# Kernel optimization log

Hardware: AMD Instinct MI355X
Metric: run time of the kernel (lower is better)

The kernel has to match this reference:

```python
import jax, jax.numpy as jnp
import numpy as np

T, B, IN_DIM, D_VALUE, D_KEY = 1024, 8, 512, 64, 64
EPS = 1e-8

def setup_inputs() -> dict:
    key = jax.random.key(0)
    ks = jax.random.split(key, 7)
    s = 1.0 / np.sqrt(IN_DIM)
    return {
        "x":  jax.random.normal(ks[0], (T, B, IN_DIM), dtype=jnp.float32),
        "Wv": jax.random.uniform(ks[1], (D_VALUE, IN_DIM), jnp.float32, -s, s),
        "bv": jax.random.uniform(ks[2], (D_VALUE,), jnp.float32, -s, s),
        "Wk": jax.random.uniform(ks[3], (D_KEY, IN_DIM), jnp.float32, -s, s),
        "bk": jax.random.uniform(ks[4], (D_KEY,), jnp.float32, -s, s),
        "Wa": jax.random.uniform(ks[5], (D_KEY, IN_DIM), jnp.float32, -s, s),
        "ba": jax.random.uniform(ks[6], (D_KEY,), jnp.float32, -s, s),
    }

def reference(x, Wv, bv, Wk, bk, Wa, ba):
    # Projections: x (T,B,in_dim) -> v (T,B,d), k (T,B,n), alpha (T,B,n)
    v = jnp.einsum('tbi,di->tbd', x, Wv) + bv
    k = jnp.einsum('tbi,ni->tbn', x, Wk) + bk
    alpha = jax.nn.sigmoid(jnp.einsum('tbi,ni->tbn', x, Wa) + ba)
    # outer product per timestep: (T,B,d,n)
    outer = jnp.einsum('tbd,tbn->tbdn', v, k)
    # log-space cumulative decay, normalized by final cumprod
    log_cumprod = jnp.cumsum(jnp.log(jnp.maximum(alpha, EPS)), axis=0)  # (T,B,n)
    cumprod = jnp.exp(log_cumprod)
    decay = cumprod / (cumprod[-1:] + EPS)
    weighted = outer * decay[:, :, None, :]  # (T,B,d,n)
    S = jnp.cumsum(weighted, axis=0)
    return S
```

## Files before the change

### kernel.cpp

```cpp
#include <hip/hip_runtime.h>
#include <math.h>

#define T_DIM  1024
#define B_DIM  8
#define IN_D   512
#define NROWS  (T_DIM * B_DIM)
#define EPSF   1e-8f

#define CHUNK  16
#define NCHUNK (T_DIM / CHUNK)
#define SEG    16
#define NSEG   (T_DIM / SEG)

typedef float vfloat4 __attribute__((ext_vector_type(4)));

#define OFF_WT   0
#define OFF_V    (OFF_WT + IN_D * 192)
#define OFF_K    (OFF_V  + NROWS * 64)
#define OFF_Z    (OFF_K  + NROWS * 64)
#define OFF_SEG  (OFF_Z  + NROWS * 64)
#define OFF_TOT  (OFF_SEG + NSEG * B_DIM * 64)
#define OFF_P    (OFF_TOT + B_DIM * 64)

__global__ void k0_wt(const float* __restrict__ Wv, const float* __restrict__ Wk,
                      const float* __restrict__ Wa, float* __restrict__ Wt) {
    int idx = blockIdx.x * 256 + threadIdx.x;
    int i = idx / 192, c = idx % 192;
    float v;
    if (c < 64)       v = Wv[c * IN_D + i];
    else if (c < 128) v = Wk[(c - 64) * IN_D + i];
    else              v = Wa[(c - 128) * IN_D + i];
    Wt[i * 192 + c] = v;
}

__global__ __launch_bounds__(256) void k1_proj(
        const float* __restrict__ x, const float* __restrict__ Wt,
        const float* __restrict__ bv, const float* __restrict__ bk, const float* __restrict__ ba,
        float* __restrict__ V, float* __restrict__ Kb, float* __restrict__ Zb) {
    __shared__ float xs[2][32][32];
    __shared__ float wsm[2][32][192];
    const int tid  = threadIdx.x;
    const int h    = tid >> 7;
    const int t7   = tid & 127;
    const int rq   = t7 >> 4;
    const int cq   = t7 & 15;
    const int row0 = blockIdx.x * 32;

    float4 acc[4][3];
#pragma unroll
    for (int j = 0; j < 4; ++j)
#pragma unroll
        for (int m = 0; m < 3; ++m) acc[j][m] = make_float4(0.f, 0.f, 0.f, 0.f);

    for (int s = 0; s < 8; ++s) {
#pragma unroll
        for (int q = 0; q < 2; ++q) {
            int idx = tid + q * 256;
            int hh = idx >> 8, r = idx & 31, f = (idx >> 5) & 7;
            float4 v4 = reinterpret_cast<const float4*>(x)[((row0 + r) * IN_D + hh * 256 + s * 32 + f * 4) >> 2];
            xs[hh][f * 4 + 0][r] = v4.x;
            xs[hh][f * 4 + 1][r] = v4.y;
            xs[hh][f * 4 + 2][r] = v4.z;
            xs[hh][f * 4 + 3][r] = v4.w;
        }
#pragma unroll
        for (int q = 0; q < 12; ++q) {
            int idx = tid + q * 256;
            int hh = idx / 1536;
            int rem = idx - hh * 1536;
            int kk = rem / 48;
            int f  = rem - kk * 48;
            float4 v4 = reinterpret_cast<const float4*>(Wt)[((hh * 256 + s * 32 + kk) * 192 + f * 4) >> 2];
            *reinterpret_cast<float4*>(&wsm[hh][kk][f * 4]) = v4;
        }
        __syncthreads();

#pragma unroll 4
        for (int kk = 0; kk < 32; ++kk) {
            float4 xv = *reinterpret_cast<const float4*>(&xs[h][kk][rq * 4]);
#pragma unroll
            for (int m = 0; m < 3; ++m) {
                float4 wq = *reinterpret_cast<const float4*>(&wsm[h][kk][m * 64 + cq * 4]);
#pragma unroll
                for (int j = 0; j < 4; ++j) {
                    float xx = (&xv.x)[j];
                    acc[j][m].x = fmaf(xx, wq.x, acc[j][m].x);
                    acc[j][m].y = fmaf(xx, wq.y, acc[j][m].y);
                    acc[j][m].z = fmaf(xx, wq.z, acc[j][m].z);
                    acc[j][m].w = fmaf(xx, wq.w, acc[j][m].w);
                }
            }
        }
        __syncthreads();
    }

    float* red = &wsm[0][0][0];
    if (h == 1) {
#pragma unroll
        for (int j = 0; j < 4; ++j)
#pragma unroll
            for (int m = 0; m < 3; ++m)
                *reinterpret_cast<float4*>(&red[t7 * 52 + (j * 3 + m) * 4]) = acc[j][m];
    }
    __syncthreads();
    if (h == 0) {
        float4 bv4 = *reinterpret_cast<const float4*>(&bv[cq * 4]);
        float4 bk4 = *reinterpret_cast<const float4*>(&bk[cq * 4]);
        float4 ba4 = *reinterpret_cast<const float4*>(&ba[cq * 4]);
#pragma unroll
        for (int j = 0; j < 4; ++j) {
            int row = row0 + rq * 4 + j;
#pragma unroll
            for (int m = 0; m < 3; ++m) {
                float4 o = *reinterpret_cast<const float4*>(&red[t7 * 52 + (j * 3 + m) * 4]);
                o.x += (&acc[j][m].x)[0];
                o.x = acc[j][m].x + (&o.x)[0] - acc[j][m].x;
            }
            float4 o0 = *reinterpret_cast<const float4*>(&red[t7 * 52 + (j * 3 + 0) * 4]);
            float4 o1 = *reinterpret_cast<const float4*>(&red[t7 * 52 + (j * 3 + 1) * 4]);
            float4 o2 = *reinterpret_cast<const float4*>(&red[t7 * 52 + (j * 3 + 2) * 4]);
            float4 r0, r1, r2;
            r0.x = acc[j][0].x + o0.x + bv4.x; r0.y = acc[j][0].y + o0.y + bv4.y;
            r0.z = acc[j][0].z + o0.z + bv4.z; r0.w = acc[j][0].w + o0.w + bv4.w;
            r1.x = acc[j][1].x + o1.x + bk4.x; r1.y = acc[j][1].y + o1.y + bk4.y;
            r1.z = acc[j][1].z + o1.z + bk4.z; r1.w = acc[j][1].w + o1.w + bk4.w;
            r2.x = acc[j][2].x + o2.x + ba4.x; r2.y = acc[j][2].y + o2.y + ba4.y;
            r2.z = acc[j][2].z + o2.z + ba4.z; r2.w = acc[j][2].w + o2.w + ba4.w;
            *reinterpret_cast<float4*>(&V [row * 64 + cq * 4]) = r0;
            *reinterpret_cast<float4*>(&Kb[row * 64 + cq * 4]) = r1;
            *reinterpret_cast<float4*>(&Zb[row * 64 + cq * 4]) = r2;
        }
    }
}

__global__ void k2a_logs(float* __restrict__ Z, float* __restrict__ seg) {
    int b = blockIdx.x & 7, s = blockIdx.x >> 3;
    int n = threadIdx.x;
    int base = b * 64 + n;
    float accv = 0.f;
#pragma unroll
    for (int i = 0; i < SEG; ++i) {
        int t = s * SEG + i;
        float z = Z[t * 512 + base];
        float a = 1.f / (1.f + expf(-z));
        float l = logf(fmaxf(a, EPSF));
        Z[t * 512 + base] = l;
        accv += l;
    }
    seg[s * 512 + base] = accv;
}

__global__ void k2b_scan(float* __restrict__ seg, float* __restrict__ tot) {
    int i = threadIdx.x;
    float vals[NSEG];
#pragma unroll
    for (int s = 0; s < NSEG; ++s) vals[s] = seg[s * 512 + i];
    float run = 0.f;
#pragma unroll
    for (int s = 0; s < NSEG; ++s) { seg[s * 512 + i] = run; run += vals[s]; }
    tot[i] = run;
}

__global__ void k2c_w(const float* __restrict__ Z, const float* __restrict__ seg,
                      const float* __restrict__ tot, float* __restrict__ Kb) {
    int b = blockIdx.x & 7, s = blockIdx.x >> 3;
    int n = threadIdx.x;
    int base = b * 64 + n;
    float run = seg[s * 512 + base];
    float invden = 1.f / (expf(tot[base]) + EPSF);
#pragma unroll
    for (int i = 0; i < SEG; ++i) {
        int t = s * SEG + i;
        run += Z[t * 512 + base];
        Kb[t * 512 + base] *= expf(run) * invden;
    }
}

__global__ __launch_bounds__(256) void k3_partial(const float* __restrict__ V,
                                                  const float* __restrict__ W,
                                                  float* __restrict__ P) {
    __shared__ float vs[CHUNK * 64];
    __shared__ float wsh[CHUNK * 64];
    int b = blockIdx.x & 7, cch = blockIdx.x >> 3;
    int tid = threadIdx.x;
    int dg = tid >> 4, n4 = tid & 15;
    {
        int il = tid >> 4, f = tid & 15;
        int row = (cch * CHUNK + il) * 8 + b;
        reinterpret_cast<float4*>(vs)[il * 16 + f]  = reinterpret_cast<const float4*>(V)[row * 16 + f];
        reinterpret_cast<float4*>(wsh)[il * 16 + f] = reinterpret_cast<const float4*>(W)[row * 16 + f];
    }
    __syncthreads();
    float4 acc[4];
#pragma unroll
    for (int q = 0; q < 4; ++q) acc[q] = make_float4(0.f, 0.f, 0.f, 0.f);

#pragma unroll
    for (int i = 0; i < CHUNK; ++i) {
        float4 wv = reinterpret_cast<const float4*>(wsh)[i * 16 + n4];
#pragma unroll
        for (int q = 0; q < 4; ++q) {
            float vd = vs[i * 64 + dg + 16 * q];
            acc[q].x = fmaf(vd, wv.x, acc[q].x);
            acc[q].y = fmaf(vd, wv.y, acc[q].y);
            acc[q].z = fmaf(vd, wv.z, acc[q].z);
            acc[q].w = fmaf(vd, wv.w, acc[q].w);
        }
    }
    float* Pp = P + (cch * 8 + b) * 4096;
#pragma unroll
    for (int q = 0; q < 4; ++q)
        *reinterpret_cast<float4*>(Pp + (dg + 16 * q) * 64 + 4 * n4) = acc[q];
}

__global__ __launch_bounds__(256) void k4_prefix(float* __restrict__ P) {
    int gid = blockIdx.x * 256 + threadIdx.x;
    int b = gid >> 12, dn = gid & 4095;
    float run = 0.f;
#pragma unroll
    for (int c = 0; c < NCHUNK; ++c) {
        float v = P[(c * 8 + b) * 4096 + dn];
        P[(c * 8 + b) * 4096 + dn] = run;
        run += v;
    }
}

__global__ __launch_bounds__(256) void k5_main(const float* __restrict__ V,
                                               const float* __restrict__ W,
                                               const float* __restrict__ P,
                                               float* __restrict__ S) {
    __shared__ float vs[CHUNK * 64];
    __shared__ float wsh[CHUNK * 64];
    int b = blockIdx.x & 7, cch = blockIdx.x >> 3;
    int tid = threadIdx.x;
    int dg = tid >> 4, n4 = tid & 15;
    {
        int il = tid >> 4, f = tid & 15;
        int row = (cch * CHUNK + il) * 8 + b;
        reinterpret_cast<float4*>(vs)[il * 16 + f]  = reinterpret_cast<const float4*>(V)[row * 16 + f];
        reinterpret_cast<float4*>(wsh)[il * 16 + f] = reinterpret_cast<const float4*>(W)[row * 16 + f];
    }
    vfloat4 acc[4];
    const float* Pp = P + (cch * 8 + b) * 4096;
#pragma unroll
    for (int q = 0; q < 4; ++q)
        acc[q] = *reinterpret_cast<const vfloat4*>(Pp + (dg + 16 * q) * 64 + 4 * n4);
    __syncthreads();

#pragma unroll
    for (int i = 0; i < CHUNK; ++i) {
        float4 wv = reinterpret_cast<const float4*>(wsh)[i * 16 + n4];
        int t = cch * CHUNK + i;
        float* Sb = S + (size_t)t * 32768 + b * 4096;
#pragma unroll
        for (int q = 0; q < 4; ++q) {
            float vd = vs[i * 64 + dg + 16 * q];
            acc[q].x = fmaf(vd, wv.x, acc[q].x);
            acc[q].y = fmaf(vd, wv.y, acc[q].y);
            acc[q].z = fmaf(vd, wv.z, acc[q].z);
            acc[q].w = fmaf(vd, wv.w, acc[q].w);
            __builtin_nontemporal_store(acc[q],
                reinterpret_cast<vfloat4*>(Sb + (dg + 16 * q) * 64 + 4 * n4));
        }
    }
}

extern "C" void kernel_launch(void* const* d_in, const int* in_sizes, int n_in,
                              void* d_out, int out_size, void* d_ws, size_t ws_size,
                              hipStream_t stream) {
    const float* x  = (const float*)d_in[0];
    const float* Wv = (const float*)d_in[1];
    const float* bv = (const float*)d_in[2];
    const float* Wk = (const float*)d_in[3];
    const float* bk = (const float*)d_in[4];
    const float* Wa = (const float*)d_in[5];
    const float* ba = (const float*)d_in[6];
    float* S  = (float*)d_out;
    float* ws = (float*)d_ws;

    float* Wt  = ws + OFF_WT;
    float* V   = ws + OFF_V;
    float* Kb  = ws + OFF_K;
    float* Zb  = ws + OFF_Z;
    float* seg = ws + OFF_SEG;
    float* tot = ws + OFF_TOT;
    float* P   = ws + OFF_P;

    k0_wt     <<<384, 256, 0, stream>>>(Wv, Wk, Wa, Wt);
    k1_proj   <<<256, 256, 0, stream>>>(x, Wt, bv, bk, ba, V, Kb, Zb);
    k2a_logs  <<<512,  64, 0, stream>>>(Zb, seg);
    k2b_scan  <<<  1, 512, 0, stream>>>(seg, tot);
    k2c_w     <<<512,  64, 0, stream>>>(Zb, seg, tot, Kb);
    k3_partial<<<512, 256, 0, stream>>>(V, Kb, P);
    k4_prefix <<<128, 256, 0, stream>>>(P);
    k5_main   <<<512, 256, 0, stream>>>(V, Kb, P, S);
}
```

Baseline: 213.7 us.

## Fuse log-sigmoid and decay scan into projection and chunk kernels

```diff
diff --git a/kernel.cpp b/kernel.cpp
--- a/kernel.cpp
+++ b/kernel.cpp
@@ -6,6 +6,7 @@
 #define IN_D   512
 #define NROWS  (T_DIM * B_DIM)
 #define EPSF   1e-8f
+#define LOG_EPS (-18.4206807f)
 
 #define CHUNK  16
 #define NCHUNK (T_DIM / CHUNK)
@@ -23,8 +24,10 @@
 #define OFF_P    (OFF_TOT + B_DIM * 64)
 
 __global__ void k0_wt(const float* __restrict__ Wv, const float* __restrict__ Wk,
-                      const float* __restrict__ Wa, float* __restrict__ Wt) {
+                      const float* __restrict__ Wa, float* __restrict__ Wt,
+                      float* __restrict__ seg) {
     int idx = blockIdx.x * 256 + threadIdx.x;
+    if (idx < NSEG * 512) seg[idx] = 0.f;
     int i = idx / 192, c = idx % 192;
     float v;
     if (c < 64)       v = Wv[c * IN_D + i];
@@ -36,7 +39,8 @@
 __global__ __launch_bounds__(256) void k1_proj(
         const float* __restrict__ x, const float* __restrict__ Wt,
         const float* __restrict__ bv, const float* __restrict__ bk, const float* __restrict__ ba,
-        float* __restrict__ V, float* __restrict__ Kb, float* __restrict__ Zb) {
+        float* __restrict__ V, float* __restrict__ Kb, float* __restrict__ Zb,
+        float* __restrict__ seg) {
     __shared__ float xs[2][32][32];
     __shared__ float wsm[2][32][192];
     const int tid  = threadIdx.x;
@@ -110,87 +114,82 @@
 #pragma unroll
         for (int j = 0; j < 4; ++j) {
             int row = row0 + rq * 4 + j;
-#pragma unroll
-            for (int m = 0; m < 3; ++m) {
-                float4 o = *reinterpret_cast<const float4*>(&red[t7 * 52 + (j * 3 + m) * 4]);
-                o.x += (&acc[j][m].x)[0];
-                o.x = acc[j][m].x + (&o.x)[0] - acc[j][m].x;
-            }
             float4 o0 = *reinterpret_cast<const float4*>(&red[t7 * 52 + (j * 3 + 0) * 4]);
             float4 o1 = *reinterpret_cast<const float4*>(&red[t7 * 52 + (j * 3 + 1) * 4]);
             float4 o2 = *reinterpret_cast<const float4*>(&red[t7 * 52 + (j * 3 + 2) * 4]);
-            float4 r0, r1, r2;
+            float4 r0, r1, z2, l4;
             r0.x = acc[j][0].x + o0.x + bv4.x; r0.y = acc[j][0].y + o0.y + bv4.y;
             r0.z = acc[j][0].z + o0.z + bv4.z; r0.w = acc[j][0].w + o0.w + bv4.w;
             r1.x = acc[j][1].x + o1.x + bk4.x; r1.y = acc[j][1].y + o1.y + bk4.y;
             r1.z = acc[j][1].z + o1.z + bk4.z; r1.w = acc[j][1].w + o1.w + bk4.w;
-            r2.x = acc[j][2].x + o2.x + ba4.x; r2.y = acc[j][2].y + o2.y + ba4.y;
-            r2.z = acc[j][2].z + o2.z + ba4.z; r2.w = acc[j][2].w + o2.w + ba4.w;
+            z2.x = acc[j][2].x + o2.x + ba4.x; z2.y = acc[j][2].y + o2.y + ba4.y;
+            z2.z = acc[j][2].z + o2.z + ba4.z; z2.w = acc[j][2].w + o2.w + ba4.w;
+            l4.x = fmaxf(-log1pf(expf(-z2.x)), LOG_EPS);
+            l4.y = fmaxf(-log1pf(expf(-z2.y)), LOG_EPS);
+            l4.z = fmaxf(-log1pf(expf(-z2.z)), LOG_EPS);
+            l4.w = fmaxf(-log1pf(expf(-z2.w)), LOG_EPS);
             *reinterpret_cast<float4*>(&V [row * 64 + cq * 4]) = r0;
             *reinterpret_cast<float4*>(&Kb[row * 64 + cq * 4]) = r1;
-            *reinterpret_cast<float4*>(&Zb[row * 64 + cq * 4]) = r2;
-        }
-    }
-}
-
-__global__ void k2a_logs(float* __restrict__ Z, float* __restrict__ seg) {
-    int b = blockIdx.x & 7, s = blockIdx.x >> 3;
-    int n = threadIdx.x;
-    int base = b * 64 + n;
-    float accv = 0.f;
-#pragma unroll
-    for (int i = 0; i < SEG; ++i) {
-        int t = s * SEG + i;
-        float z = Z[t * 512 + base];
-        float a = 1.f / (1.f + expf(-z));
-        float l = logf(fmaxf(a, EPSF));
-        Z[t * 512 + base] = l;
-        accv += l;
-    }
-    seg[s * 512 + base] = accv;
-}
-
-__global__ void k2b_scan(float* __restrict__ seg, float* __restrict__ tot) {
-    int i = threadIdx.x;
-    float vals[NSEG];
-#pragma unroll
-    for (int s = 0; s < NSEG; ++s) vals[s] = seg[s * 512 + i];
-    float run = 0.f;
-#pragma unroll
-    for (int s = 0; s < NSEG; ++s) { seg[s * 512 + i] = run; run += vals[s]; }
-    tot[i] = run;
-}
-
-__global__ void k2c_w(const float* __restrict__ Z, const float* __restrict__ seg,
-                      const float* __restrict__ tot, float* __restrict__ Kb) {
-    int b = blockIdx.x & 7, s = blockIdx.x >> 3;
-    int n = threadIdx.x;
-    int base = b * 64 + n;
-    float run = seg[s * 512 + base];
-    float invden = 1.f / (expf(tot[base]) + EPSF);
-#pragma unroll
-    for (int i = 0; i < SEG; ++i) {
-        int t = s * SEG + i;
-        run += Z[t * 512 + base];
-        Kb[t * 512 + base] *= expf(run) * invden;
-    }
-}
+            *reinterpret_cast<float4*>(&Zb[row * 64 + cq * 4]) = l4;
+            int sg = row >> 7;
+            float* sp = &seg[sg * 512 + (row & 7) * 64 + cq * 4];
+            atomicAdd(sp + 0, l4.x);
+            atomicAdd(sp + 1, l4.y);
+            atomicAdd(sp + 2, l4.z);
+            atomicAdd(sp + 3, l4.w);
+        }
+    }
+}
+
 
 __global__ __launch_bounds__(256) void k3_partial(const float* __restrict__ V,
-                                                  const float* __restrict__ W,
+                                                  const float* __restrict__ Z,
+                                                  const float* __restrict__ seg,
+                                                  const float* __restrict__ Kb,
                                                   float* __restrict__ P) {
     __shared__ float vs[CHUNK * 64];
     __shared__ float wsh[CHUNK * 64];
+    __shared__ float gsum[4 * 64];
     int b = blockIdx.x & 7, cch = blockIdx.x >> 3;
     int tid = threadIdx.x;
     int dg = tid >> 4, n4 = tid & 15;
-    {
-        int il = tid >> 4, f = tid & 15;
-        int row = (cch * CHUNK + il) * 8 + b;
-        reinterpret_cast<float4*>(vs)[il * 16 + f]  = reinterpret_cast<const float4*>(V)[row * 16 + f];
-        reinterpret_cast<float4*>(wsh)[il * 16 + f] = reinterpret_cast<const float4*>(W)[row * 16 + f];
-    }
-    __syncthreads();
+    int n = tid & 63, g = tid >> 6;
+    int base = b * 64 + n;
+
+    int il = tid >> 4, f = tid & 15;
+    float4 v4 = reinterpret_cast<const float4*>(V)[((cch * CHUNK + il) * 8 + b) * 16 + f];
+
+    float run = 0.f, total = 0.f;
+#pragma unroll 8
+    for (int s2 = 0; s2 < NSEG; ++s2) {
+        float sv = seg[s2 * 512 + base];
+        if (s2 < cch) run += sv;
+        total += sv;
+    }
+    float invden = 1.f / (expf(total) + EPSF);
+
+    int t0 = cch * CHUNK + g * 4;
+    float l0 = Z[(t0 + 0) * 512 + base];
+    float l1 = Z[(t0 + 1) * 512 + base];
+    float l2 = Z[(t0 + 2) * 512 + base];
+    float l3 = Z[(t0 + 3) * 512 + base];
+    float k0v = Kb[(t0 + 0) * 512 + base];
+    float k1v = Kb[(t0 + 1) * 512 + base];
+    float k2v = Kb[(t0 + 2) * 512 + base];
+    float k3v = Kb[(t0 + 3) * 512 + base];
+    gsum[g * 64 + n] = l0 + l1 + l2 + l3;
+    reinterpret_cast<float4*>(vs)[il * 16 + f] = v4;
+    __syncthreads();
+    float pre = run;
+#pragma unroll
+    for (int g2 = 0; g2 < 3; ++g2) if (g2 < g) pre += gsum[g2 * 64 + n];
+    float c0 = pre + l0, c1 = c0 + l1, c2 = c1 + l2, c3 = c2 + l3;
+    wsh[(g * 4 + 0) * 64 + n] = k0v * expf(c0) * invden;
+    wsh[(g * 4 + 1) * 64 + n] = k1v * expf(c1) * invden;
+    wsh[(g * 4 + 2) * 64 + n] = k2v * expf(c2) * invden;
+    wsh[(g * 4 + 3) * 64 + n] = k3v * expf(c3) * invden;
+    __syncthreads();
+
     float4 acc[4];
 #pragma unroll
     for (int q = 0; q < 4; ++q) acc[q] = make_float4(0.f, 0.f, 0.f, 0.f);
@@ -226,25 +225,57 @@
 }
 
 __global__ __launch_bounds__(256) void k5_main(const float* __restrict__ V,
-                                               const float* __restrict__ W,
+                                               const float* __restrict__ Z,
+                                               const float* __restrict__ seg,
+                                               const float* __restrict__ Kb,
                                                const float* __restrict__ P,
                                                float* __restrict__ S) {
     __shared__ float vs[CHUNK * 64];
     __shared__ float wsh[CHUNK * 64];
+    __shared__ float gsum[4 * 64];
     int b = blockIdx.x & 7, cch = blockIdx.x >> 3;
     int tid = threadIdx.x;
     int dg = tid >> 4, n4 = tid & 15;
-    {
-        int il = tid >> 4, f = tid & 15;
-        int row = (cch * CHUNK + il) * 8 + b;
-        reinterpret_cast<float4*>(vs)[il * 16 + f]  = reinterpret_cast<const float4*>(V)[row * 16 + f];
-        reinterpret_cast<float4*>(wsh)[il * 16 + f] = reinterpret_cast<const float4*>(W)[row * 16 + f];
-    }
+    int n = tid & 63, g = tid >> 6;
+    int base = b * 64 + n;
+
+    int il = tid >> 4, f = tid & 15;
+    float4 v4 = reinterpret_cast<const float4*>(V)[((cch * CHUNK + il) * 8 + b) * 16 + f];
     vfloat4 acc[4];
     const float* Pp = P + (cch * 8 + b) * 4096;
 #pragma unroll
     for (int q = 0; q < 4; ++q)
         acc[q] = *reinterpret_cast<const vfloat4*>(Pp + (dg + 16 * q) * 64 + 4 * n4);
+
+    float run = 0.f, total = 0.f;
+#pragma unroll 8
+    for (int s2 = 0; s2 < NSEG; ++s2) {
+        float sv = seg[s2 * 512 + base];
+        if (s2 < cch) run += sv;
+        total += sv;
+    }
+    float invden = 1.f / (expf(total) + EPSF);
+
+    int t0 = cch * CHUNK + g * 4;
+    float l0 = Z[(t0 + 0) * 512 + base];
+    float l1 = Z[(t0 + 1) * 512 + base];
+    float l2 = Z[(t0 + 2) * 512 + base];
+    float l3 = Z[(t0 + 3) * 512 + base];
+    float k0v = Kb[(t0 + 0) * 512 + base];
+    float k1v = Kb[(t0 + 1) * 512 + base];
+    float k2v = Kb[(t0 + 2) * 512 + base];
+    float k3v = Kb[(t0 + 3) * 512 + base];
+    gsum[g * 64 + n] = l0 + l1 + l2 + l3;
+    reinterpret_cast<float4*>(vs)[il * 16 + f] = v4;
+    __syncthreads();
+    float pre = run;
+#pragma unroll
+    for (int g2 = 0; g2 < 3; ++g2) if (g2 < g) pre += gsum[g2 * 64 + n];
+    float c0 = pre + l0, c1 = c0 + l1, c2 = c1 + l2, c3 = c2 + l3;
+    wsh[(g * 4 + 0) * 64 + n] = k0v * expf(c0) * invden;
+    wsh[(g * 4 + 1) * 64 + n] = k1v * expf(c1) * invden;
+    wsh[(g * 4 + 2) * 64 + n] = k2v * expf(c2) * invden;
+    wsh[(g * 4 + 3) * 64 + n] = k3v * expf(c3) * invden;
     __syncthreads();
 
 #pragma unroll
@@ -283,15 +314,11 @@
     float* Kb  = ws + OFF_K;
     float* Zb  = ws + OFF_Z;
     float* seg = ws + OFF_SEG;
-    float* tot = ws + OFF_TOT;
     float* P   = ws + OFF_P;
 
-    k0_wt     <<<384, 256, 0, stream>>>(Wv, Wk, Wa, Wt);
-    k1_proj   <<<256, 256, 0, stream>>>(x, Wt, bv, bk, ba, V, Kb, Zb);
-    k2a_logs  <<<512,  64, 0, stream>>>(Zb, seg);
-    k2b_scan  <<<  1, 512, 0, stream>>>(seg, tot);
-    k2c_w     <<<512,  64, 0, stream>>>(Zb, seg, tot, Kb);
-    k3_partial<<<512, 256, 0, stream>>>(V, Kb, P);
+    k0_wt     <<<384, 256, 0, stream>>>(Wv, Wk, Wa, Wt, seg);
+    k1_proj   <<<256, 256, 0, stream>>>(x, Wt, bv, bk, ba, V, Kb, Zb, seg);
+    k3_partial<<<512, 256, 0, stream>>>(V, Zb, seg, Kb, P);
     k4_prefix <<<128, 256, 0, stream>>>(P);
-    k5_main   <<<512, 256, 0, stream>>>(V, Kb, P, S);
-}
+    k5_main   <<<512, 256, 0, stream>>>(V, Zb, seg, Kb, P, S);
+}
```

Measured after the change: 216.4 us. About the same (+1.3%).
